# Optimization experiments

Measured on AMD Instinct MI355X. Metric: run time of the kernel, lower is better.

Reference implementation:

```python
import jax, jax.numpy as jnp
import numpy as np

VIS_DIM, TXT_DIM, HID = 2048, 1024, 1024


def setup_inputs() -> dict:
    key = jax.random.key(0)
    ks = jax.random.split(key, 8)
    def lin(kw, kb, fan_in, fan_out):
        bound = 1.0 / np.sqrt(fan_in)
        W = jax.random.uniform(kw, (fan_out, fan_in), jnp.float32, -bound, bound)
        b = jax.random.uniform(kb, (fan_out,), jnp.float32, -bound, bound)
        return W, b
    Wv, bv = lin(ks[0], ks[1], VIS_DIM, HID)
    Wt, bt = lin(ks[2], ks[3], TXT_DIM, HID)
    Wa, ba = lin(ks[4], ks[5], HID, 1)
    return {
        "visual_features": jax.random.normal(ks[6], (128, 256, VIS_DIM), jnp.float32),
        "text_features": jax.random.normal(ks[7], (128, TXT_DIM), jnp.float32),
        "Wv": Wv, "bv": bv, "Wt": Wt, "bt": bt, "Wa": Wa, "ba": ba,
    }


def reference(visual_features, text_features, Wv, bv, Wt, bt, Wa, ba):
    # v: (B, R, H); t: (B, 1, H) broadcast over regions
    v = jnp.einsum("brd,hd->brh", visual_features, Wv) + bv
    t = (text_features @ Wt.T + bt)[:, None, :]
    combined = jnp.tanh(v + t)                       # (B, R, H)
    scores = jnp.einsum("brh,h->br", combined, Wa[0]) + ba[0]  # (B, R)
    attention_weights = jax.nn.softmax(scores, axis=1)
    attended = jnp.einsum("br,brd->bd", attention_weights, visual_features)
    return attended, attention_weights
```

## Files before the change

kernel.cpp:

```cpp
#include <hip/hip_runtime.h>
#include <hip/hip_bf16.h>

#define VIS_DIM 2048
#define TXT_DIM 1024
#define HID     1024
#define NB      128
#define NR      256
#define M_TOT   (NB*NR)

#define N_ATILES 8192
#define N_TILES  8448
#define TILE_B   16384
#define TSTRIDE  (32 * TILE_B)
#define WS_SCORES_OFF ((size_t)N_TILES * TILE_B)
#define WS_NEED (WS_SCORES_OFF + 131072 + 524288)

typedef __attribute__((ext_vector_type(4))) float  f32x4;
typedef __attribute__((ext_vector_type(8))) short  short8;
typedef __attribute__((ext_vector_type(4))) unsigned short u16x4;

static __device__ __forceinline__ unsigned short f2bf(float f) {
    union { __hip_bfloat16 h; unsigned short u; } c;
    c.h = __float2bfloat16(f);
    return c.u;
}

static __device__ __forceinline__ float tanh_fast(float x) {
    float xc = fminf(fmaxf(x, -15.f), 15.f);
    float e  = __expf(2.f * xc);
    return (e - 1.f) / (e + 1.f);
}

__global__ void init_ws(float* __restrict__ scores, float* __restrict__ tbuf,
                        const float* __restrict__ bt) {
    int i = blockIdx.x * 256 + threadIdx.x;
    if (i < M_TOT) scores[i] = 0.f;
    tbuf[i] = bt[i & (HID - 1)];
}

__global__ __launch_bounds__(256) void prepass(const float* __restrict__ A,
                                               const float* __restrict__ Bv,
                                               unsigned short* __restrict__ w16) {
    const int t   = blockIdx.x;
    const int tid = threadIdx.x;
    const int mb  = (t < N_ATILES ? t : t - N_ATILES) >> 5;
    const int kt  = t & 31;
    const float* src = (t < N_ATILES ? A : Bv) + (size_t)mb * 128 * VIS_DIM + kt * 64;
    unsigned short* dst = w16 + (size_t)t * (TILE_B / 2);
    #pragma unroll
    for (int i = 0; i < 4; ++i) {
        int si = i * 256 + tid;
        int row = si >> 3, slot = si & 7;
        const float* p = src + (size_t)row * VIS_DIM + slot * 8;
        f32x4 lo = *(const f32x4*)p;
        f32x4 hi = *(const f32x4*)(p + 4);
        short8 v;
        v[0] = (short)f2bf(lo.x); v[1] = (short)f2bf(lo.y);
        v[2] = (short)f2bf(lo.z); v[3] = (short)f2bf(lo.w);
        v[4] = (short)f2bf(hi.x); v[5] = (short)f2bf(hi.y);
        v[6] = (short)f2bf(hi.z); v[7] = (short)f2bf(hi.w);
        *(short8*)(dst + row * 64 + ((slot ^ (row & 7)) << 3)) = v;
    }
}

__global__ __launch_bounds__(256) void gemm_text(const float* __restrict__ text,
                                                 const float* __restrict__ Wt,
                                                 float* __restrict__ tbuf) {
    __shared__ float As[128][33];
    __shared__ float Bs[32][33];
    const int n0  = blockIdx.x * 32;
    const int k0  = blockIdx.y * 256;
    const int tid = threadIdx.x;
    const int tm  = tid >> 3;
    const int tn  = tid & 7;
    float acc[4][4] = {};
    for (int kt = 0; kt < 8; ++kt) {
        const int k = k0 + kt * 32;
        {
            int row = tid >> 1, off = (tid & 1) * 16;
            const float* src = text + row * TXT_DIM + k + off;
            #pragma unroll
            for (int j = 0; j < 4; ++j) {
                f32x4 v = *(const f32x4*)(src + j * 4);
                As[row][off + j*4 + 0] = v.x; As[row][off + j*4 + 1] = v.y;
                As[row][off + j*4 + 2] = v.z; As[row][off + j*4 + 3] = v.w;
            }
        }
        {
            int row = tid >> 3, off = (tid & 7) * 4;
            f32x4 v = *(const f32x4*)(Wt + (size_t)(n0 + row) * TXT_DIM + k + off);
            Bs[row][off + 0] = v.x; Bs[row][off + 1] = v.y;
            Bs[row][off + 2] = v.z; Bs[row][off + 3] = v.w;
        }
        __syncthreads();
        #pragma unroll
        for (int kk = 0; kk < 32; ++kk) {
            float a[4], b[4];
            #pragma unroll
            for (int i = 0; i < 4; ++i) a[i] = As[tm*4 + i][kk];
            #pragma unroll
            for (int j = 0; j < 4; ++j) b[j] = Bs[tn*4 + j][kk];
            #pragma unroll
            for (int i = 0; i < 4; ++i)
                #pragma unroll
                for (int j = 0; j < 4; ++j) acc[i][j] += a[i] * b[j];
        }
        __syncthreads();
    }
    #pragma unroll
    for (int i = 0; i < 4; ++i)
        #pragma unroll
        for (int j = 0; j < 4; ++j)
            atomicAdd(&tbuf[(tm*4 + i) * HID + n0 + tn*4 + j], acc[i][j]);
}

static __device__ __forceinline__ int toff(int row, int kElem) {
    return row * 128 + ((((kElem >> 3) & 7) ^ (row & 7)) << 4);
}

__global__ __launch_bounds__(512, 2) void gemm_256(
        const unsigned short* __restrict__ w16,
        const float* __restrict__ bv,
        const float* __restrict__ wa,
        const float* __restrict__ tbuf,
        float* __restrict__ scores) {
    __shared__ __align__(16) char lds[131072];

    const int wg   = blockIdx.x;
    const int xcd  = wg & 7;
    const int loc  = wg >> 3;
    const int mb   = xcd * 16 + (loc >> 2);
    const int nb   = loc & 3;
    const int brow = mb * 256;
    const int bcol = nb * 256;

    const int tid  = threadIdx.x;
    const int lane = tid & 63;
    const int wid  = tid >> 6;
    const int wr   = wid >> 2;
    const int wc   = wid & 3;
    const int l    = lane & 15, g = lane >> 4;

    const char* wb = (const char*)w16;
    const char* pA = wb + (size_t)(2 * mb) * TSTRIDE + wid * 1024 + lane * 16;
    const char* pB = wb + (size_t)N_ATILES * TILE_B
                        + (size_t)(2 * nb) * TSTRIDE + wid * 1024 + lane * 16;

    f32x4 acc[8][4] = {};

#define GLOADS(koff, bufbase)                                                  \
    do {                                                                       \
        _Pragma("unroll")                                                      \
        for (int j = 0; j < 8; ++j) {                                          \
            const char* s_ = (j < 4                                            \
                ? pA + (j >> 1) * (size_t)TSTRIDE + (j & 1) * 8192             \
                : pB + ((j - 4) >> 1) * (size_t)TSTRIDE + ((j - 4) & 1) * 8192)\
                + (koff);                                                      \
            __builtin_amdgcn_global_load_lds(                                  \
                (const __attribute__((address_space(1))) float*)s_,            \
                (__attribute__((address_space(3))) float*)                     \
                    (lds + (bufbase) + j * 8192 + wid * 1024),                 \
                16, 0, 0);                                                     \
        }                                                                      \
    } while (0)

#define VWAIT0()                                                               \
    do {                                                                       \
        __builtin_amdgcn_sched_barrier(0);                                     \
        asm volatile("s_waitcnt vmcnt(0)" ::: "memory");                       \
        __builtin_amdgcn_sched_barrier(0);                                     \
    } while (0)

#define BARRIER()                                                              \
    do {                                                                       \
        __builtin_amdgcn_sched_barrier(0);                                     \
        asm volatile("s_waitcnt lgkmcnt(0)" ::: "memory");                     \
        __builtin_amdgcn_s_barrier();                                          \
        __builtin_amdgcn_sched_barrier(0);                                     \
    } while (0)

#define PHASE(bufbase, s)                                                      \
    do {                                                                       \
        const int kE = (s) * 32 + g * 8;                                       \
        const char* pa_ = lds + (bufbase) + wr * 16384;                        \
        const char* pb_ = lds + (bufbase) + 32768 + (wc >> 1) * 16384;         \
        short8 bfr[4];                                                         \
        _Pragma("unroll")                                                      \
        for (int n = 0; n < 4; ++n)                                            \
            bfr[n] = *(const short8*)(pb_ + toff((wc & 1) * 64 + n * 16 + l, kE)); \
        _Pragma("unroll")                                                      \
        for (int m = 0; m < 8; ++m) {                                          \
            short8 af = *(const short8*)(pa_ + toff(m * 16 + l, kE));          \
            acc[m][0] = __builtin_amdgcn_mfma_f32_16x16x32_bf16(af, bfr[0], acc[m][0], 0, 0, 0); \
            acc[m][1] = __builtin_amdgcn_mfma_f32_16x16x32_bf16(af, bfr[1], acc[m][1], 0, 0, 0); \
            acc[m][2] = __builtin_amdgcn_mfma_f32_16x16x32_bf16(af, bfr[2], acc[m][2], 0, 0, 0); \
            acc[m][3] = __builtin_amdgcn_mfma_f32_16x16x32_bf16(af, bfr[3], acc[m][3], 0, 0, 0); \
        }                                                                      \
    } while (0)

    GLOADS((size_t)0, 0);
    VWAIT0();
    GLOADS((size_t)TILE_B, 65536);
    BARRIER();

    #pragma unroll 1
    for (int i = 0; i < 16; ++i) {
        const size_t k2 = (size_t)(2 * i + 2) * TILE_B;
        PHASE(0, 0);
        PHASE(0, 1);
        VWAIT0();
        BARRIER();
        if (i < 15) GLOADS(k2, 0);
        PHASE(65536, 0);
        PHASE(65536, 1);
        if (i < 15) {
            VWAIT0();
            BARRIER();
            GLOADS(k2 + TILE_B, 65536);
        }
    }
#undef GLOADS
#undef VWAIT0
#undef BARRIER
#undef PHASE

    const int b = mb;
    float wa_c[4], bvt_c[4];
    #pragma unroll
    for (int n = 0; n < 4; ++n) {
        int col = bcol + wc * 64 + n * 16 + l;
        wa_c[n]  = wa[col];
        bvt_c[n] = bv[col] + tbuf[b * HID + col];
    }
    #pragma unroll
    for (int m = 0; m < 8; ++m) {
        float p0 = 0.f, p1 = 0.f, p2 = 0.f, p3 = 0.f;
        #pragma unroll
        for (int n = 0; n < 4; ++n) {
            f32x4 v = acc[m][n];
            p0 += wa_c[n] * tanh_fast(v.x + bvt_c[n]);
            p1 += wa_c[n] * tanh_fast(v.y + bvt_c[n]);
            p2 += wa_c[n] * tanh_fast(v.z + bvt_c[n]);
            p3 += wa_c[n] * tanh_fast(v.w + bvt_c[n]);
        }
        #pragma unroll
        for (int d = 1; d < 16; d <<= 1) {
            p0 += __shfl_xor(p0, d); p1 += __shfl_xor(p1, d);
            p2 += __shfl_xor(p2, d); p3 += __shfl_xor(p3, d);
        }
        if ((lane & 15) == 0) {
            int rowg = brow + wr * 128 + m * 16 + g * 4;
            atomicAdd(&scores[rowg + 0], p0);
            atomicAdd(&scores[rowg + 1], p1);
            atomicAdd(&scores[rowg + 2], p2);
            atomicAdd(&scores[rowg + 3], p3);
        }
    }
}

#define BK 32
#define NT (VIS_DIM / BK)

static __device__ __forceinline__ int tile_off(int row, int kElem) {
    return row * 64 + (((kElem >> 3) ^ ((row >> 1) & 3)) << 4);
}

__global__ __launch_bounds__(256, 2) void gemm_vis(
        const float* __restrict__ A,
        const float* __restrict__ Bv,
        const float* __restrict__ bv,
        const float* __restrict__ wa,
        const float* __restrict__ tbuf,
        float* __restrict__ scores) {
    __shared__ __align__(16) char lds[32768];

    const int wg   = blockIdx.x;
    const int xcd  = wg & 7;
    const int loc  = wg >> 3;
    const int mb   = xcd * 32 + (loc >> 3);
    const int nb   = loc & 7;
    const int brow = mb * 128;
    const int bcol = nb * 128;

    const int tid  = threadIdx.x;
    const int lane = tid & 63;
    const int wid  = tid >> 6;
    const int wr   = wid >> 1, wc = wid & 1;

    const int srow = tid >> 3;
    const int sfs  = tid & 7;
    unsigned va0 = ((unsigned)(brow + srow      ) * VIS_DIM + sfs * 4) * 4u;
    unsigned va1 = va0 + 32u * VIS_DIM * 4u;
    unsigned va2 = va0 + 64u * VIS_DIM * 4u;
    unsigned va3 = va0 + 96u * VIS_DIM * 4u;
    unsigned vb0 = ((unsigned)(bcol + srow      ) * VIS_DIM + sfs * 4) * 4u;
    unsigned vb1 = vb0 + 32u * VIS_DIM * 4u;
    unsigned vb2 = vb0 + 64u * VIS_DIM * 4u;
    unsigned vb3 = vb0 + 96u * VIS_DIM * 4u;

    int wbyte[4];
    #pragma unroll
    for (int r = 0; r < 4; ++r) {
        int row = srow + 32 * r;
        wbyte[r] = row * 64 + (((sfs >> 1) ^ ((row >> 1) & 3)) << 4) + (sfs & 1) * 8;
    }

    f32x4 sA0, sA1, sA2, sA3, sB0, sB1, sB2, sB3;
    f32x4 tA0, tA1, tA2, tA3, tB0, tB1, tB2, tB3;
    f32x4 acc[4][4] = {};

#define GLOAD_SET(dA0,dA1,dA2,dA3,dB0,dB1,dB2,dB3)                             \
    do {                                                                       \
        asm volatile("global_load_dwordx4 %0, %1, %2"                          \
                     : "=&v"(dA0) : "v"(va0), "s"(A) : "memory");              \
        asm volatile("global_load_dwordx4 %0, %1, %2"                          \
                     : "=&v"(dA1) : "v"(va1), "s"(A) : "memory");              \
        asm volatile("global_load_dwordx4 %0, %1, %2"                          \
                     : "=&v"(dA2) : "v"(va2), "s"(A) : "memory");              \
        asm volatile("global_load_dwordx4 %0, %1, %2"                          \
                     : "=&v"(dA3) : "v"(va3), "s"(A) : "memory");              \
        asm volatile("global_load_dwordx4 %0, %1, %2"                          \
                     : "=&v"(dB0) : "v"(vb0), "s"(Bv) : "memory");             \
        asm volatile("global_load_dwordx4 %0, %1, %2"                          \
                     : "=&v"(dB1) : "v"(vb1), "s"(Bv) : "memory");             \
        asm volatile("global_load_dwordx4 %0, %1, %2"                          \
                     : "=&v"(dB2) : "v"(vb2), "s"(Bv) : "memory");             \
        asm volatile("global_load_dwordx4 %0, %1, %2"                          \
                     : "=&v"(dB3) : "v"(vb3), "s"(Bv) : "memory");             \
        va0 += BK * 4; va1 += BK * 4; va2 += BK * 4; va3 += BK * 4;            \
        vb0 += BK * 4; vb1 += BK * 4; vb2 += BK * 4; vb3 += BK * 4;            \
    } while (0)

#define GLOAD_S() GLOAD_SET(sA0,sA1,sA2,sA3,sB0,sB1,sB2,sB3)
#define GLOAD_T() GLOAD_SET(tA0,tA1,tA2,tA3,tB0,tB1,tB2,tB3)

#define VWAIT(N)                                                               \
    do {                                                                       \
        __builtin_amdgcn_sched_barrier(0);                                     \
        asm volatile("s_waitcnt vmcnt(" #N ")" ::: "memory");                  \
        __builtin_amdgcn_sched_barrier(0);                                     \
    } while (0)

#define BARRIER()                                                              \
    do {                                                                       \
        __builtin_amdgcn_sched_barrier(0);                                     \
        asm volatile("s_waitcnt lgkmcnt(0)" ::: "memory");                     \
        __builtin_amdgcn_s_barrier();                                          \
        __builtin_amdgcn_sched_barrier(0);                                     \
    } while (0)

#define CVT8(dst, v0)                                                          \
    do {                                                                       \
        u16x4 t_;                                                              \
        t_.x = f2bf((v0).x); t_.y = f2bf((v0).y);                              \
        t_.z = f2bf((v0).z); t_.w = f2bf((v0).w);                              \
        dst = t_;                                                              \
    } while (0)

#define LWRITE_SET(bufbase, dA0,dA1,dA2,dA3,dB0,dB1,dB2,dB3)                   \
    do {                                                                       \
        u16x4 w_;                                                              \
        char* la = lds + (bufbase);                                            \
        char* lb = lds + (bufbase) + 8192;                                     \
        CVT8(w_, dA0); *(u16x4*)(la + wbyte[0]) = w_;                          \
        CVT8(w_, dA1); *(u16x4*)(la + wbyte[1]) = w_;                          \
        CVT8(w_, dA2); *(u16x4*)(la + wbyte[2]) = w_;                          \
        CVT8(w_, dA3); *(u16x4*)(la + wbyte[3]) = w_;                          \
        CVT8(w_, dB0); *(u16x4*)(lb + wbyte[0]) = w_;                          \
        CVT8(w_, dB1); *(u16x4*)(lb + wbyte[1]) = w_;                          \
        CVT8(w_, dB2); *(u16x4*)(lb + wbyte[2]) = w_;                          \
        CVT8(w_, dB3); *(u16x4*)(lb + wbyte[3]) = w_;                          \
    } while (0)

#define LWRITE_S(bufbase) LWRITE_SET(bufbase, sA0,sA1,sA2,sA3,sB0,sB1,sB2,sB3)
#define LWRITE_T(bufbase) LWRITE_SET(bufbase, tA0,tA1,tA2,tA3,tB0,tB1,tB2,tB3)

#define COMPUTE(bufbase)                                                       \
    do {                                                                       \
        short8 af[4], bf[4];                                                   \
        const int kk = (lane >> 4) * 8;                                        \
        const char* la = lds + (bufbase);                                      \
        const char* lb = lds + (bufbase) + 8192;                               \
        _Pragma("unroll")                                                      \
        for (int m = 0; m < 4; ++m)                                            \
            af[m] = *(const short8*)(la + tile_off(wr*64 + m*16 + (lane&15), kk)); \
        _Pragma("unroll")                                                      \
        for (int n = 0; n < 4; ++n)                                            \
            bf[n] = *(const short8*)(lb + tile_off(wc*64 + n*16 + (lane&15), kk)); \
        _Pragma("unroll")                                                      \
        for (int m = 0; m < 4; ++m)                                            \
            _Pragma("unroll")                                                  \
            for (int n = 0; n < 4; ++n)                                        \
                acc[m][n] = __builtin_amdgcn_mfma_f32_16x16x32_bf16(           \
                    af[m], bf[n], acc[m][n], 0, 0, 0);                         \
    } while (0)

    GLOAD_S();
    GLOAD_T();
    VWAIT(8);
    LWRITE_S(0);
    BARRIER();

    #pragma unroll 1
    for (int kt = 0; kt < NT - 2; kt += 2) {
        GLOAD_S();
        COMPUTE(0);
        VWAIT(8);
        LWRITE_T(16384);
        BARRIER();
        GLOAD_T();
        COMPUTE(16384);
        VWAIT(8);
        LWRITE_S(0);
        BARRIER();
    }
    COMPUTE(0);
    VWAIT(0);
    LWRITE_T(16384);
    BARRIER();
    COMPUTE(16384);
#undef GLOAD_SET
#undef GLOAD_S
#undef GLOAD_T
#undef VWAIT
#undef BARRIER
#undef CVT8
#undef LWRITE_SET
#undef LWRITE_S
#undef LWRITE_T
#undef COMPUTE

    const int b = brow >> 8;
    float wa_c[4], bvt_c[4];
    #pragma unroll
    for (int n = 0; n < 4; ++n) {
        int col = bcol + wc * 64 + n * 16 + (lane & 15);
        wa_c[n]  = wa[col];
        bvt_c[n] = bv[col] + tbuf[b * HID + col];
    }
    #pragma unroll
    for (int m = 0; m < 4; ++m) {
        float p0 = 0.f, p1 = 0.f, p2 = 0.f, p3 = 0.f;
        #pragma unroll
        for (int n = 0; n < 4; ++n) {
            f32x4 v = acc[m][n];
            p0 += wa_c[n] * tanh_fast(v.x + bvt_c[n]);
            p1 += wa_c[n] * tanh_fast(v.y + bvt_c[n]);
            p2 += wa_c[n] * tanh_fast(v.z + bvt_c[n]);
            p3 += wa_c[n] * tanh_fast(v.w + bvt_c[n]);
        }
        #pragma unroll
        for (int d = 1; d < 16; d <<= 1) {
            p0 += __shfl_xor(p0, d); p1 += __shfl_xor(p1, d);
            p2 += __shfl_xor(p2, d); p3 += __shfl_xor(p3, d);
        }
        if ((lane & 15) == 0) {
            int rowg = brow + wr * 64 + m * 16 + (lane >> 4) * 4;
            atomicAdd(&scores[rowg + 0], p0);
            atomicAdd(&scores[rowg + 1], p1);
            atomicAdd(&scores[rowg + 2], p2);
            atomicAdd(&scores[rowg + 3], p3);
        }
    }
}

__global__ __launch_bounds__(256) void attend(const float* __restrict__ visual,
                                              const float* __restrict__ scores,
                                              float* __restrict__ out) {
    const int chunk = blockIdx.x;
    const int b     = blockIdx.y;
    const int tid   = threadIdx.x;
    const int lane  = tid & 63;
    const int wv    = tid >> 6;

    __shared__ float wsm[NR];
    __shared__ float red[4];
    __shared__ f32x4 part[4][64];

    float s = scores[b * NR + tid];
    float mx = s;
    #pragma unroll
    for (int d = 1; d < 64; d <<= 1) mx = fmaxf(mx, __shfl_xor(mx, d));
    if (lane == 0) red[wv] = mx;
    __syncthreads();
    mx = fmaxf(fmaxf(red[0], red[1]), fmaxf(red[2], red[3]));
    float e = __expf(s - mx);
    float sum = e;
    #pragma unroll
    for (int d = 1; d < 64; d <<= 1) sum += __shfl_xor(sum, d);
    __syncthreads();
    if (lane == 0) red[wv] = sum;
    __syncthreads();
    sum = red[0] + red[1] + red[2] + red[3];
    float w = e * (1.f / sum);
    wsm[tid] = w;
    if (chunk == 0) out[(size_t)NB * VIS_DIM + b * NR + tid] = w;
    __syncthreads();

    const float* vb = visual + ((size_t)b * NR + wv * 64) * VIS_DIM + chunk * 256 + lane * 4;
    f32x4 acc = {0.f, 0.f, 0.f, 0.f};
    #pragma unroll
    for (int r = 0; r < 64; r += 4) {
        f32x4 v0 = *(const f32x4*)(vb + (size_t)(r + 0) * VIS_DIM);
        f32x4 v1 = *(const f32x4*)(vb + (size_t)(r + 1) * VIS_DIM);
        f32x4 v2 = *(const f32x4*)(vb + (size_t)(r + 2) * VIS_DIM);
        f32x4 v3 = *(const f32x4*)(vb + (size_t)(r + 3) * VIS_DIM);
        acc += wsm[wv * 64 + r + 0] * v0;
        acc += wsm[wv * 64 + r + 1] * v1;
        acc += wsm[wv * 64 + r + 2] * v2;
        acc += wsm[wv * 64 + r + 3] * v3;
    }
    part[wv][lane] = acc;
    __syncthreads();
    if (wv == 0) {
        f32x4 a = part[0][lane] + part[1][lane] + part[2][lane] + part[3][lane];
        *(f32x4*)(out + (size_t)b * VIS_DIM + chunk * 256 + lane * 4) = a;
    }
}

extern "C" void kernel_launch(void* const* d_in, const int* in_sizes, int n_in,
                              void* d_out, int out_size, void* d_ws, size_t ws_size,
                              hipStream_t stream) {
    (void)in_sizes; (void)n_in; (void)out_size;
    const float* visual = (const float*)d_in[0];
    const float* text   = (const float*)d_in[1];
    const float* Wv     = (const float*)d_in[2];
    const float* bv     = (const float*)d_in[3];
    const float* Wt     = (const float*)d_in[4];
    const float* bt     = (const float*)d_in[5];
    const float* Wa     = (const float*)d_in[6];

    float* out = (float*)d_out;
    const bool fast = ws_size >= (size_t)WS_NEED;

    if (fast) {
        unsigned short* w16 = (unsigned short*)d_ws;
        float* scores = (float*)((char*)d_ws + WS_SCORES_OFF);
        float* tbuf   = scores + M_TOT;
        prepass  <<<N_TILES, 256, 0, stream>>>(visual, Wv, w16);
        init_ws  <<<512, 256, 0, stream>>>(scores, tbuf, bt);
        gemm_text<<<dim3(32, 4), 256, 0, stream>>>(text, Wt, tbuf);
        gemm_256 <<<512, 512, 0, stream>>>(w16, bv, Wa, tbuf, scores);
        attend   <<<dim3(8, NB), 256, 0, stream>>>(visual, scores, out);
    } else {
        float* scores = (float*)d_ws;
        float* tbuf   = scores + M_TOT;
        init_ws  <<<512, 256, 0, stream>>>(scores, tbuf, bt);
        gemm_text<<<dim3(32, 4), 256, 0, stream>>>(text, Wt, tbuf);
        gemm_vis <<<2048, 256, 0, stream>>>(visual, Wv, bv, Wa, tbuf, scores);
        attend   <<<dim3(8, NB), 256, 0, stream>>>(visual, scores, out);
    }
}
```

Baseline: 270.7 us.

## Read bf16 tiled visual copy in attend and batch A-fragment loads with MFMA priority

The final weighted-sum kernel now reads the bf16 tiled copy of the visual features already produced by the prepass, using the swizzled tile addressing, instead of re-reading the fp32 input. This halves the bytes loaded in the attend stage. The GEMM inner phase also preloads all A fragments before issuing MFMAs and raises wave priority around the MFMA block to improve issue overlap. The output is now computed from bf16-rounded features, so it loses precision relative to the fp32 reference.

```diff
diff --git a/kernel.cpp b/kernel.cpp
--- a/kernel.cpp
+++ b/kernel.cpp
@@ -23,6 +23,10 @@
     union { __hip_bfloat16 h; unsigned short u; } c;
     c.h = __float2bfloat16(f);
     return c.u;
+}
+
+static __device__ __forceinline__ float bf2f(unsigned short u) {
+    union { float f; unsigned u; } c; c.u = ((unsigned)u) << 16; return c.f;
 }
 
 static __device__ __forceinline__ float tanh_fast(float x) {
@@ -184,18 +188,22 @@
         const int kE = (s) * 32 + g * 8;                                       \
         const char* pa_ = lds + (bufbase) + wr * 16384;                        \
         const char* pb_ = lds + (bufbase) + 32768 + (wc >> 1) * 16384;         \
-        short8 bfr[4];                                                         \
+        short8 bfr[4], afr[8];                                                 \
         _Pragma("unroll")                                                      \
         for (int n = 0; n < 4; ++n)                                            \
             bfr[n] = *(const short8*)(pb_ + toff((wc & 1) * 64 + n * 16 + l, kE)); \
         _Pragma("unroll")                                                      \
+        for (int m = 0; m < 8; ++m)                                            \
+            afr[m] = *(const short8*)(pa_ + toff(m * 16 + l, kE));             \
+        __builtin_amdgcn_s_setprio(1);                                         \
+        _Pragma("unroll")                                                      \
         for (int m = 0; m < 8; ++m) {                                          \
-            short8 af = *(const short8*)(pa_ + toff(m * 16 + l, kE));          \
-            acc[m][0] = __builtin_amdgcn_mfma_f32_16x16x32_bf16(af, bfr[0], acc[m][0], 0, 0, 0); \
-            acc[m][1] = __builtin_amdgcn_mfma_f32_16x16x32_bf16(af, bfr[1], acc[m][1], 0, 0, 0); \
-            acc[m][2] = __builtin_amdgcn_mfma_f32_16x16x32_bf16(af, bfr[2], acc[m][2], 0, 0, 0); \
-            acc[m][3] = __builtin_amdgcn_mfma_f32_16x16x32_bf16(af, bfr[3], acc[m][3], 0, 0, 0); \
+            acc[m][0] = __builtin_amdgcn_mfma_f32_16x16x32_bf16(afr[m], bfr[0], acc[m][0], 0, 0, 0); \
+            acc[m][1] = __builtin_amdgcn_mfma_f32_16x16x32_bf16(afr[m], bfr[1], acc[m][1], 0, 0, 0); \
+            acc[m][2] = __builtin_amdgcn_mfma_f32_16x16x32_bf16(afr[m], bfr[2], acc[m][2], 0, 0, 0); \
+            acc[m][3] = __builtin_amdgcn_mfma_f32_16x16x32_bf16(afr[m], bfr[3], acc[m][3], 0, 0, 0); \
         }                                                                      \
+        __builtin_amdgcn_s_setprio(0);                                         \
     } while (0)
 
     GLOADS((size_t)0, 0);
@@ -255,6 +263,82 @@
             atomicAdd(&scores[rowg + 2], p2);
             atomicAdd(&scores[rowg + 3], p3);
         }
+    }
+}
+
+__global__ __launch_bounds__(256) void attend_bf16(
+        const unsigned short* __restrict__ w16,
+        const float* __restrict__ scores,
+        float* __restrict__ out) {
+    const int chunk = blockIdx.x;
+    const int b     = blockIdx.y;
+    const int tid   = threadIdx.x;
+    const int lane  = tid & 63;
+    const int wv    = tid >> 6;
+
+    __shared__ float wsm[NR];
+    __shared__ float red[4];
+    __shared__ float part2[4][32][8];
+
+    float s = scores[b * NR + tid];
+    float mx = s;
+    #pragma unroll
+    for (int d = 1; d < 64; d <<= 1) mx = fmaxf(mx, __shfl_xor(mx, d));
+    if (lane == 0) red[wv] = mx;
+    __syncthreads();
+    mx = fmaxf(fmaxf(red[0], red[1]), fmaxf(red[2], red[3]));
+    float e = __expf(s - mx);
+    float sum = e;
+    #pragma unroll
+    for (int d = 1; d < 64; d <<= 1) sum += __shfl_xor(sum, d);
+    __syncthreads();
+    if (lane == 0) red[wv] = sum;
+    __syncthreads();
+    sum = red[0] + red[1] + red[2] + red[3];
+    float w = e * (1.f / sum);
+    wsm[tid] = w;
+    if (chunk == 0) out[(size_t)NB * VIS_DIM + b * NR + tid] = w;
+    __syncthreads();
+
+    const int half  = lane >> 5;
+    const int dslot = lane & 31;
+    const int d0    = chunk * 256 + dslot * 8;
+    const int kt    = d0 >> 6;
+    const int ksl   = (d0 >> 3) & 7;
+    const int rbase = b * 256 + wv * 64 + half;
+
+    float acc[8] = {};
+    #pragma unroll 4
+    for (int step = 0; step < 32; ++step) {
+        int rowg = rbase + step * 2;
+        const char* p = (const char*)w16
+            + ((size_t)(rowg >> 7) * 32 + kt) * TILE_B
+            + (rowg & 127) * 128 + ((ksl ^ (rowg & 7)) << 4);
+        short8 v = *(const short8*)p;
+        float w_ = wsm[wv * 64 + step * 2 + half];
+        #pragma unroll
+        for (int j = 0; j < 8; ++j)
+            acc[j] += w_ * bf2f((unsigned short)v[j]);
+    }
+    #pragma unroll
+    for (int j = 0; j < 8; ++j) acc[j] += __shfl_xor(acc[j], 32);
+
+    if (half == 0) {
+        #pragma unroll
+        for (int j = 0; j < 8; ++j) part2[wv][dslot][j] = acc[j];
+    }
+    __syncthreads();
+    if (wv == 0 && half == 0) {
+        float o[8];
+        #pragma unroll
+        for (int j = 0; j < 8; ++j)
+            o[j] = part2[0][dslot][j] + part2[1][dslot][j]
+                 + part2[2][dslot][j] + part2[3][dslot][j];
+        float* dst = out + (size_t)b * VIS_DIM + chunk * 256 + dslot * 8;
+        f32x4 lo = {o[0], o[1], o[2], o[3]};
+        f32x4 hi = {o[4], o[5], o[6], o[7]};
+        *(f32x4*)dst = lo;
+        *(f32x4*)(dst + 4) = hi;
     }
 }
 
@@ -537,11 +621,11 @@
         unsigned short* w16 = (unsigned short*)d_ws;
         float* scores = (float*)((char*)d_ws + WS_SCORES_OFF);
         float* tbuf   = scores + M_TOT;
-        prepass  <<<N_TILES, 256, 0, stream>>>(visual, Wv, w16);
-        init_ws  <<<512, 256, 0, stream>>>(scores, tbuf, bt);
-        gemm_text<<<dim3(32, 4), 256, 0, stream>>>(text, Wt, tbuf);
-        gemm_256 <<<512, 512, 0, stream>>>(w16, bv, Wa, tbuf, scores);
-        attend   <<<dim3(8, NB), 256, 0, stream>>>(visual, scores, out);
+        prepass    <<<N_TILES, 256, 0, stream>>>(visual, Wv, w16);
+        init_ws    <<<512, 256, 0, stream>>>(scores, tbuf, bt);
+        gemm_text  <<<dim3(32, 4), 256, 0, stream>>>(text, Wt, tbuf);
+        gemm_256   <<<512, 512, 0, stream>>>(w16, bv, Wa, tbuf, scores);
+        attend_bf16<<<dim3(8, NB), 256, 0, stream>>>(w16, scores, out);
     } else {
         float* scores = (float*)d_ws;
         float* tbuf   = scores + M_TOT;
```

Result: faster. 247.3 us (-8.6%).
